# Optimization experiments

Hardware: AMD Instinct MI355X
Metric: run time of the kernel (lower is better)

The kernel has to match this reference:

```python
import jax, jax.numpy as jnp
import numpy as np
from jax.ops import segment_sum

N_NODES = 100000
N_EDGES = 1600000
IN_DIM, HID_DIM, OUT_DIM = 64, 48, 32


def setup_inputs() -> dict:
    key = jax.random.key(0)
    ks = jax.random.split(key, 4)
    x = jax.random.normal(ks[0], (N_NODES, IN_DIM), dtype=jnp.float32)
    edge_index = jax.random.randint(ks[1], (2, N_EDGES), 0, N_NODES, dtype=jnp.int64)
    W1 = jax.random.normal(ks[2], (IN_DIM, HID_DIM), dtype=jnp.float32) / np.sqrt(IN_DIM)
    b1 = jnp.zeros((HID_DIM,), dtype=jnp.float32)
    W2 = jax.random.normal(ks[3], (HID_DIM, OUT_DIM), dtype=jnp.float32) / np.sqrt(HID_DIM)
    b2 = jnp.zeros((OUT_DIM,), dtype=jnp.float32)
    return {"x": x, "edge_index": edge_index, "W1": W1, "b1": b1, "W2": W2, "b2": b2}


def _gcn_conv(x, W, b, src, dst, deg_inv_sqrt, n_nodes):
    # GCNConv: out = D^{-1/2} (A + I) D^{-1/2} (x W) + b
    h = x @ W                                   # [N, F_out]
    norm = deg_inv_sqrt[src] * deg_inv_sqrt[dst]  # [E+N]
    msg = h[src] * norm[:, None]                # gather + scale
    out = segment_sum(msg, dst, num_segments=n_nodes)  # scatter-add over dst
    return out + b


def reference(x, edge_index, W1, b1, W2, b2):
    n = x.shape[0]
    loop = jnp.arange(n, dtype=edge_index.dtype)
    src = jnp.concatenate([edge_index[0], loop])  # add self-loops (PyG default)
    dst = jnp.concatenate([edge_index[1], loop])
    deg = segment_sum(jnp.ones_like(dst, dtype=x.dtype), dst, num_segments=n)
    deg_inv_sqrt = jnp.where(deg > 0, jax.lax.rsqrt(jnp.maximum(deg, 1.0)), 0.0)
    h = _gcn_conv(x, W1, b1, src, dst, deg_inv_sqrt, n)
    h = jax.nn.relu(h)
    embeddings = _gcn_conv(h, W2, b2, src, dst, deg_inv_sqrt, n)
    return embeddings
```

## Files before the change

### kernel.cpp

```cpp
#include <hip/hip_runtime.h>
#include <hip/hip_fp16.h>


#define NN 100000
#define NE 1600000
#define NPB 128
#define NBUCK ((NN + NPB - 1) / NPB)
#define PBITS 17
#define PMASK ((1 << PBITS) - 1)
#define CHB 3
#define CHS 14
#define NKEY (NPB << CHB)
#define CAP 4096
#define UN 8
#define PART_B 512
#define EPT 8
#define PART_G ((NE + PART_B * EPT - 1) / (PART_B * EPT))
#define GROWS 256
#define GEMM_G ((NN + GROWS - 1) / GROWS)
#define GB NBUCK

struct alignas(8)  half4 { __half2 lo, hi; };
struct alignas(16) half8 { __half2 a, b, c, d; };

__global__ __launch_bounds__(512) void
k_partgemm(const int* __restrict__ src, const int* __restrict__ dst,
           int* __restrict__ cursor, int* __restrict__ packed,
           const float* __restrict__ X, const float* __restrict__ W1,
           __half* __restrict__ Hh) {
    __shared__ int h[NBUCK];
    __shared__ int base_[NBUCK];
    __shared__ float w[64 * 48];
    int tid = threadIdx.x;

    if (blockIdx.x < PART_G) {
        for (int i = tid; i < NBUCK; i += PART_B) h[i] = 0;
        __syncthreads();
        int ebase = blockIdx.x * (PART_B * EPT);
        for (int k = 0; k < EPT; ++k) {
            int e = ebase + k * PART_B + tid;
            if (e < NE) atomicAdd(&h[dst[e] >> 7], 1);
        }
        __syncthreads();
        for (int i = tid; i < NBUCK; i += PART_B) {
            int c = h[i];
            if (c) base_[i] = atomicAdd(&cursor[i], c);
            h[i] = 0;
        }
        __syncthreads();
        for (int k = 0; k < EPT; ++k) {
            int e = ebase + k * PART_B + tid;
            if (e < NE) {
                int d = dst[e];
                int b = d >> 7;
                int r = atomicAdd(&h[b], 1);
                packed[(size_t)b * CAP + base_[b] + r] = src[e] | ((d & (NPB - 1)) << PBITS);
            }
        }
        return;
    }

    constexpr int NC = 48, CPT = 12, CG = 4, KF4 = 16;
    int R0 = (blockIdx.x - PART_G) * GROWS;
    for (int i = tid; i < 64 * 48; i += 512) w[i] = W1[i];
    __syncthreads();

    int tc = tid % CG, tr = tid / CG;
    int r0 = R0 + 2 * tr, r1 = r0 + 1;
    int c0 = tc * CPT;
    bool ok0 = r0 < NN, ok1 = r1 < NN;
    const float4* X4 = (const float4*)X;
    const float4 z4 = make_float4(0.f, 0.f, 0.f, 0.f);

    float acc[2][CPT];
#pragma unroll
    for (int rr = 0; rr < 2; ++rr)
#pragma unroll
        for (int j = 0; j < CPT; ++j) acc[rr][j] = 0.f;

#pragma unroll 2
    for (int k4 = 0; k4 < KF4; ++k4) {
        float4 xa = ok0 ? X4[(size_t)r0 * KF4 + k4] : z4;
        float4 xb = ok1 ? X4[(size_t)r1 * KF4 + k4] : z4;
        float ar[4] = {xa.x, xa.y, xa.z, xa.w};
        float br[4] = {xb.x, xb.y, xb.z, xb.w};
#pragma unroll
        for (int j = 0; j < 4; ++j) {
            float va = ar[j], vb = br[j];
#pragma unroll
            for (int q = 0; q < CPT / 4; ++q) {
                float4 wv = *(const float4*)&w[(4 * k4 + j) * NC + c0 + 4 * q];
                acc[0][q*4+0] = fmaf(va, wv.x, acc[0][q*4+0]);
                acc[0][q*4+1] = fmaf(va, wv.y, acc[0][q*4+1]);
                acc[0][q*4+2] = fmaf(va, wv.z, acc[0][q*4+2]);
                acc[0][q*4+3] = fmaf(va, wv.w, acc[0][q*4+3]);
                acc[1][q*4+0] = fmaf(vb, wv.x, acc[1][q*4+0]);
                acc[1][q*4+1] = fmaf(vb, wv.y, acc[1][q*4+1]);
                acc[1][q*4+2] = fmaf(vb, wv.z, acc[1][q*4+2]);
                acc[1][q*4+3] = fmaf(vb, wv.w, acc[1][q*4+3]);
            }
        }
    }
#pragma unroll
    for (int rr = 0; rr < 2; ++rr) {
        int gr = r0 + rr;
        if (gr >= NN) continue;
#pragma unroll
        for (int q = 0; q < CPT / 4; ++q) {
            __half2 p0 = __floats2half2_rn(acc[rr][q*4+0], acc[rr][q*4+1]);
            __half2 p1 = __floats2half2_rn(acc[rr][q*4+2], acc[rr][q*4+3]);
            half4 hv; hv.lo = p0; hv.hi = p1;
            *(half4*)(Hh + (size_t)gr * NC + c0 + 4 * q) = hv;
        }
    }
}

__global__ void k_bsort(const int* __restrict__ packed, const int* __restrict__ cursor,
                        int* __restrict__ srcsort, unsigned int* __restrict__ rowinfo,
                        float* __restrict__ dinv) {
    __shared__ int stage[CAP];
    __shared__ int cnt[NKEY];
    __shared__ int tsum[256];
    int tid = threadIdx.x, b = blockIdx.x;
    int e0 = b * CAP, sz = cursor[b];
    for (int i = tid; i < NKEY; i += 256) cnt[i] = 0;
    __syncthreads();
    for (int i = tid; i < sz; i += 256) {
        int w = packed[e0 + i];
        stage[i] = w;
        int key = ((w >> PBITS) << CHB) | ((w & PMASK) >> CHS);
        atomicAdd(&cnt[key], 1);
    }
    __syncthreads();
    int k0 = tid * 4;
    int c0 = cnt[k0], c1 = cnt[k0 + 1], c2 = cnt[k0 + 2], c3 = cnt[k0 + 3];
    int loc = c0 + c1 + c2 + c3;
    tsum[tid] = loc;
    __syncthreads();
    for (int off = 1; off < 256; off <<= 1) {
        int v = (tid >= off) ? tsum[tid - off] : 0;
        __syncthreads();
        tsum[tid] += v;
        __syncthreads();
    }
    int base = tsum[tid] - loc;
    cnt[k0]     = base;
    cnt[k0 + 1] = base + c0;
    cnt[k0 + 2] = base + c0 + c1;
    cnt[k0 + 3] = base + c0 + c1 + c2;
    __syncthreads();
    if (tid < NPB) {
        int node = b * NPB + tid;
        int rs = cnt[tid << CHB];
        int re = (tid == NPB - 1) ? sz : cnt[(tid + 1) << CHB];
        if (node < NN) {
            rowinfo[node] = ((unsigned int)(e0 + rs) << 10) | (unsigned int)(re - rs);
            dinv[node] = rsqrtf((float)(re - rs + 1));
        }
    }
    __syncthreads();
    for (int i = tid; i < sz; i += 256) {
        int w = stage[i];
        int key = ((w >> PBITS) << CHB) | ((w & PMASK) >> CHS);
        int p = atomicAdd(&cnt[key], 1);
        srcsort[e0 + p] = w & PMASK;
    }
}

__global__ __launch_bounds__(256) void
k_fused48(const __half* __restrict__ Hh, const unsigned int* __restrict__ rowinfo,
          const int* __restrict__ srcsort, const float* __restrict__ dinv,
          const float* __restrict__ b1, const float* __restrict__ W2,
          __half* __restrict__ Hh2) {
    constexpr int ROWS = 128, XS = 49;
    __shared__ float Xs[ROWS * XS];
    __shared__ float w2[48 * 32];
    __shared__ float bb[48];
    int tid = threadIdx.x;
    int R0 = blockIdx.x * ROWS;
    for (int i = tid; i < 48 * 32; i += 256) w2[i] = W2[i];
    if (tid < 48) bb[tid] = b1[tid];
    __syncthreads();

    for (int t = tid; t < ROWS * 6; t += 256) {
        int lr = t / 6, q = t - lr * 6;
        int r = R0 + lr;
        if (r >= NN) continue;
        float dself = dinv[r];
        half8 sv = *(const half8*)(Hh + (size_t)r * 48 + 8 * q);
        float2 f0 = __half22float2(sv.a), f1 = __half22float2(sv.b);
        float2 f2 = __half22float2(sv.c), f3 = __half22float2(sv.d);
        float a0 = f0.x * dself, a1 = f0.y * dself;
        float a2 = f1.x * dself, a3 = f1.y * dself;
        float a4 = f2.x * dself, a5 = f2.y * dself;
        float a6 = f3.x * dself, a7 = f3.y * dself;
        unsigned int rp = rowinfo[r];
        int e0 = rp >> 10, e1 = e0 + (int)(rp & 1023);
        for (int e = e0; e < e1; e += UN) {
            int ss[UN]; float ms[UN];
#pragma unroll
            for (int u = 0; u < UN; ++u) {
                int ee = e + u;
                bool ok = ee < e1;
                ss[u] = srcsort[ok ? ee : e0];
                ms[u] = ok ? 1.f : 0.f;
            }
            half8 vv[UN]; float dv[UN];
#pragma unroll
            for (int u = 0; u < UN; ++u) {
                vv[u] = *(const half8*)(Hh + (size_t)ss[u] * 48 + 8 * q);
                dv[u] = dinv[ss[u]];
            }
#pragma unroll
            for (int u = 0; u < UN; ++u) {
                float2 g0 = __half22float2(vv[u].a), g1 = __half22float2(vv[u].b);
                float2 g2 = __half22float2(vv[u].c), g3 = __half22float2(vv[u].d);
                float m = ms[u] * dv[u];
                a0 = fmaf(g0.x, m, a0); a1 = fmaf(g0.y, m, a1);
                a2 = fmaf(g1.x, m, a2); a3 = fmaf(g1.y, m, a3);
                a4 = fmaf(g2.x, m, a4); a5 = fmaf(g2.y, m, a5);
                a6 = fmaf(g3.x, m, a6); a7 = fmaf(g3.y, m, a7);
            }
        }
        float d = dself;
        float* xr = &Xs[lr * XS + 8 * q];
        const float* bf = &bb[8 * q];
        xr[0] = fmaxf(fmaf(a0, d, bf[0]), 0.f);
        xr[1] = fmaxf(fmaf(a1, d, bf[1]), 0.f);
        xr[2] = fmaxf(fmaf(a2, d, bf[2]), 0.f);
        xr[3] = fmaxf(fmaf(a3, d, bf[3]), 0.f);
        xr[4] = fmaxf(fmaf(a4, d, bf[4]), 0.f);
        xr[5] = fmaxf(fmaf(a5, d, bf[5]), 0.f);
        xr[6] = fmaxf(fmaf(a6, d, bf[6]), 0.f);
        xr[7] = fmaxf(fmaf(a7, d, bf[7]), 0.f);
    }
    __syncthreads();

    int tc = tid & 3, tr = tid >> 2;
    int r0l = 2 * tr, c0 = tc * 8;
    float acc[2][8];
#pragma unroll
    for (int rr = 0; rr < 2; ++rr)
#pragma unroll
        for (int j = 0; j < 8; ++j) acc[rr][j] = 0.f;
#pragma unroll 4
    for (int k = 0; k < 48; ++k) {
        float x0 = Xs[r0l * XS + k];
        float x1 = Xs[(r0l + 1) * XS + k];
        float4 wv0 = *(const float4*)&w2[k * 32 + c0];
        float4 wv1 = *(const float4*)&w2[k * 32 + c0 + 4];
        acc[0][0] = fmaf(x0, wv0.x, acc[0][0]); acc[0][1] = fmaf(x0, wv0.y, acc[0][1]);
        acc[0][2] = fmaf(x0, wv0.z, acc[0][2]); acc[0][3] = fmaf(x0, wv0.w, acc[0][3]);
        acc[0][4] = fmaf(x0, wv1.x, acc[0][4]); acc[0][5] = fmaf(x0, wv1.y, acc[0][5]);
        acc[0][6] = fmaf(x0, wv1.z, acc[0][6]); acc[0][7] = fmaf(x0, wv1.w, acc[0][7]);
        acc[1][0] = fmaf(x1, wv0.x, acc[1][0]); acc[1][1] = fmaf(x1, wv0.y, acc[1][1]);
        acc[1][2] = fmaf(x1, wv0.z, acc[1][2]); acc[1][3] = fmaf(x1, wv0.w, acc[1][3]);
        acc[1][4] = fmaf(x1, wv1.x, acc[1][4]); acc[1][5] = fmaf(x1, wv1.y, acc[1][5]);
        acc[1][6] = fmaf(x1, wv1.z, acc[1][6]); acc[1][7] = fmaf(x1, wv1.w, acc[1][7]);
    }
#pragma unroll
    for (int rr = 0; rr < 2; ++rr) {
        int gr = R0 + r0l + rr;
        if (gr >= NN) continue;
        float d = dinv[gr];
        __half2 p0 = __floats2half2_rn(acc[rr][0] * d, acc[rr][1] * d);
        __half2 p1 = __floats2half2_rn(acc[rr][2] * d, acc[rr][3] * d);
        __half2 p2 = __floats2half2_rn(acc[rr][4] * d, acc[rr][5] * d);
        __half2 p3 = __floats2half2_rn(acc[rr][6] * d, acc[rr][7] * d);
        half8 hv; hv.a = p0; hv.b = p1; hv.c = p2; hv.d = p3;
        *(half8*)(Hh2 + (size_t)gr * 32 + c0) = hv;
    }
}

template <int NC>
__global__ void k_agg(const __half* __restrict__ Hh, const unsigned int* __restrict__ rowinfo,
                      const int* __restrict__ srcsort, const float* __restrict__ dinv,
                      const float* __restrict__ bias, float* __restrict__ out) {
    constexpr int Q = NC / 8;
    int idx = blockIdx.x * blockDim.x + threadIdx.x;
    if (idx >= NN * Q) return;
    int r = idx / Q, q = idx - r * Q;
    half8 sv = *(const half8*)(Hh + (size_t)r * NC + 8 * q);
    float2 f0 = __half22float2(sv.a), f1 = __half22float2(sv.b);
    float2 f2 = __half22float2(sv.c), f3 = __half22float2(sv.d);
    float a0 = f0.x, a1 = f0.y, a2 = f1.x, a3 = f1.y;
    float a4 = f2.x, a5 = f2.y, a6 = f3.x, a7 = f3.y;
    unsigned int rp = rowinfo[r];
    int e0 = rp >> 10, e1 = e0 + (int)(rp & 1023);
    for (int e = e0; e < e1; e += UN) {
        int ss[UN]; float ms[UN];
#pragma unroll
        for (int u = 0; u < UN; ++u) {
            int ee = e + u;
            bool ok = ee < e1;
            ss[u] = srcsort[ok ? ee : e0];
            ms[u] = ok ? 1.f : 0.f;
        }
        half8 vv[UN];
#pragma unroll
        for (int u = 0; u < UN; ++u)
            vv[u] = *(const half8*)(Hh + (size_t)ss[u] * NC + 8 * q);
#pragma unroll
        for (int u = 0; u < UN; ++u) {
            float2 g0 = __half22float2(vv[u].a), g1 = __half22float2(vv[u].b);
            float2 g2 = __half22float2(vv[u].c), g3 = __half22float2(vv[u].d);
            float m = ms[u];
            a0 = fmaf(g0.x, m, a0); a1 = fmaf(g0.y, m, a1);
            a2 = fmaf(g1.x, m, a2); a3 = fmaf(g1.y, m, a3);
            a4 = fmaf(g2.x, m, a4); a5 = fmaf(g2.y, m, a5);
            a6 = fmaf(g3.x, m, a6); a7 = fmaf(g3.y, m, a7);
        }
    }
    float d = dinv[r];
    const float4* b4 = (const float4*)bias;
    float4 bv0 = b4[2 * q], bv1 = b4[2 * q + 1];
    a0 = fmaf(a0, d, bv0.x); a1 = fmaf(a1, d, bv0.y);
    a2 = fmaf(a2, d, bv0.z); a3 = fmaf(a3, d, bv0.w);
    a4 = fmaf(a4, d, bv1.x); a5 = fmaf(a5, d, bv1.y);
    a6 = fmaf(a6, d, bv1.z); a7 = fmaf(a7, d, bv1.w);
    float4* o4 = (float4*)(out + (size_t)r * NC + 8 * q);
    o4[0] = make_float4(a0, a1, a2, a3);
    o4[1] = make_float4(a4, a5, a6, a7);
}

extern "C" void kernel_launch(void* const* d_in, const int* in_sizes, int n_in,
                              void* d_out, int out_size, void* d_ws, size_t ws_size,
                              hipStream_t stream) {
    const float* x  = (const float*)d_in[0];
    const int*   ei = (const int*)d_in[1];
    const float* W1 = (const float*)d_in[2];
    const float* b1 = (const float*)d_in[3];
    const float* W2 = (const float*)d_in[4];
    const float* b2 = (const float*)d_in[5];
    float* out = (float*)d_out;

    const int* src = ei;
    const int* dst = ei + NE;

    char* p = (char*)d_ws;
    auto take = [&](size_t elems) { void* q = p; p += ((elems * 4 + 255) & ~255ull); return q; };
    int*          cursor  = (int*)take(NBUCK);
    unsigned int* rowinfo = (unsigned int*)take(NN);
    float*        dinv    = (float*)take(NN);
    int*          srcsort = (int*)take((size_t)NBUCK * CAP);
    __half*       Hh      = (__half*)take((size_t)NN * 24);
    int*          packed  = (int*)take((size_t)NBUCK * CAP);
    __half*       Hh2     = (__half*)packed;

    const int B = 256;
    hipMemsetAsync(cursor, 0, NBUCK * sizeof(int), stream);
    k_partgemm<<<PART_G + GEMM_G, 512, 0, stream>>>(src, dst, cursor, packed, x, W1, Hh);
    k_bsort<<<NBUCK, 256, 0, stream>>>(packed, cursor, srcsort, rowinfo, dinv);
    k_fused48<<<GB, 256, 0, stream>>>(Hh, rowinfo, srcsort, dinv, b1, W2, Hh2);
    k_agg<32><<<(NN * 4 + B - 1) / B, B, 0, stream>>>(Hh2, rowinfo, srcsort, dinv, b2, out);
}
```

Baseline: 205.9 us.

## Replace atomic bucket scatter with per-block local sort runs and segment merge

The partition kernel no longer reserves space with global atomics on a bucket cursor and scatters each edge to a random global slot. Each block now sorts its edges by bucket locally in shared memory, writes them out as one contiguous run, and records a per-bucket offset and length table. The bucket-sort kernel then gathers its bucket's segments from all runs into shared memory before the counting sort. This removes the global atomics, the memset and the scattered writes, but each bucket block now makes many short serial per-thread segment reads, and the new seg table adds extra memory traffic.

```diff
diff --git a/kernel.cpp b/kernel.cpp
--- a/kernel.cpp
+++ b/kernel.cpp
@@ -15,7 +15,8 @@
 #define UN 8
 #define PART_B 512
 #define EPT 8
-#define PART_G ((NE + PART_B * EPT - 1) / (PART_B * EPT))
+#define RUNW (PART_B * EPT)
+#define PART_G ((NE + RUNW - 1) / RUNW)
 #define GROWS 256
 #define GEMM_G ((NN + GROWS - 1) / GROWS)
 #define GB NBUCK
@@ -24,39 +25,62 @@
 struct alignas(16) half8 { __half2 a, b, c, d; };
 
 __global__ __launch_bounds__(512) void
-k_partgemm(const int* __restrict__ src, const int* __restrict__ dst,
-           int* __restrict__ cursor, int* __restrict__ packed,
-           const float* __restrict__ X, const float* __restrict__ W1,
-           __half* __restrict__ Hh) {
+k_lsortgemm(const int* __restrict__ src, const int* __restrict__ dst,
+            int* __restrict__ runs, unsigned int* __restrict__ seg,
+            const float* __restrict__ X, const float* __restrict__ W1,
+            __half* __restrict__ Hh) {
     __shared__ int h[NBUCK];
-    __shared__ int base_[NBUCK];
+    __shared__ int tsum[512];
+    __shared__ int stage[RUNW];
     __shared__ float w[64 * 48];
     int tid = threadIdx.x;
 
     if (blockIdx.x < PART_G) {
         for (int i = tid; i < NBUCK; i += PART_B) h[i] = 0;
         __syncthreads();
-        int ebase = blockIdx.x * (PART_B * EPT);
-        for (int k = 0; k < EPT; ++k) {
-            int e = ebase + k * PART_B + tid;
-            if (e < NE) atomicAdd(&h[dst[e] >> 7], 1);
-        }
-        __syncthreads();
-        for (int i = tid; i < NBUCK; i += PART_B) {
-            int c = h[i];
-            if (c) base_[i] = atomicAdd(&cursor[i], c);
-            h[i] = 0;
-        }
-        __syncthreads();
+        int ebase = blockIdx.x * RUNW;
+        int pw[EPT], pb[EPT];
+#pragma unroll
         for (int k = 0; k < EPT; ++k) {
             int e = ebase + k * PART_B + tid;
             if (e < NE) {
                 int d = dst[e];
-                int b = d >> 7;
-                int r = atomicAdd(&h[b], 1);
-                packed[(size_t)b * CAP + base_[b] + r] = src[e] | ((d & (NPB - 1)) << PBITS);
+                pb[k] = d >> 7;
+                pw[k] = src[e] | ((d & (NPB - 1)) << PBITS);
+                atomicAdd(&h[pb[k]], 1);
+            } else pb[k] = -1;
+        }
+        __syncthreads();
+        int c0 = 0, c1 = 0;
+        if (tid < NBUCK / 2) { c0 = h[2 * tid]; c1 = h[2 * tid + 1]; }
+        int loc = c0 + c1;
+        tsum[tid] = (tid < NBUCK / 2) ? loc : 0;
+        __syncthreads();
+        for (int off = 1; off < 512; off <<= 1) {
+            int v = (tid >= off) ? tsum[tid - off] : 0;
+            __syncthreads();
+            tsum[tid] += v;
+            __syncthreads();
+        }
+        if (tid < NBUCK / 2) {
+            int base = tsum[tid] - loc;
+            seg[(size_t)blockIdx.x * NBUCK + 2 * tid]     = ((unsigned)base << 9) | (unsigned)c0;
+            seg[(size_t)blockIdx.x * NBUCK + 2 * tid + 1] = ((unsigned)(base + c0) << 9) | (unsigned)c1;
+            h[2 * tid]     = base;
+            h[2 * tid + 1] = base + c0;
+        }
+        __syncthreads();
+#pragma unroll
+        for (int k = 0; k < EPT; ++k) {
+            if (pb[k] >= 0) {
+                int r = atomicAdd(&h[pb[k]], 1);
+                stage[r] = pw[k];
             }
         }
+        __syncthreads();
+#pragma unroll
+        for (int k = 0; k < EPT; ++k)
+            runs[(size_t)blockIdx.x * RUNW + k * PART_B + tid] = stage[k * PART_B + tid];
         return;
     }
 
@@ -115,19 +139,40 @@
     }
 }
 
-__global__ void k_bsort(const int* __restrict__ packed, const int* __restrict__ cursor,
-                        int* __restrict__ srcsort, unsigned int* __restrict__ rowinfo,
-                        float* __restrict__ dinv) {
+__global__ __launch_bounds__(256) void
+k_bsort2(const int* __restrict__ runs, const unsigned int* __restrict__ seg,
+         int* __restrict__ srcsort, unsigned int* __restrict__ rowinfo,
+         float* __restrict__ dinv) {
     __shared__ int stage[CAP];
     __shared__ int cnt[NKEY];
     __shared__ int tsum[256];
     int tid = threadIdx.x, b = blockIdx.x;
-    int e0 = b * CAP, sz = cursor[b];
+
+    unsigned int s0 = (tid < PART_G) ? seg[(size_t)tid * NBUCK + b] : 0u;
+    unsigned int s1 = (tid + 256 < PART_G) ? seg[(size_t)(tid + 256) * NBUCK + b] : 0u;
+    int l0 = (int)(s0 & 511u), l1 = (int)(s1 & 511u);
+    int mylen = l0 + l1;
+    tsum[tid] = mylen;
+    __syncthreads();
+    for (int off = 1; off < 256; off <<= 1) {
+        int v = (tid >= off) ? tsum[tid - off] : 0;
+        __syncthreads();
+        tsum[tid] += v;
+        __syncthreads();
+    }
+    int wbase = tsum[tid] - mylen;
+    int sz = tsum[255];
+    {
+        const int* p = runs + (size_t)tid * RUNW + (s0 >> 9);
+        for (int i = 0; i < l0; ++i) stage[wbase + i] = p[i];
+        p = runs + (size_t)(tid + 256) * RUNW + (s1 >> 9);
+        for (int i = 0; i < l1; ++i) stage[wbase + l0 + i] = p[i];
+    }
     for (int i = tid; i < NKEY; i += 256) cnt[i] = 0;
     __syncthreads();
+
     for (int i = tid; i < sz; i += 256) {
-        int w = packed[e0 + i];
-        stage[i] = w;
+        int w = stage[i];
         int key = ((w >> PBITS) << CHB) | ((w & PMASK) >> CHS);
         atomicAdd(&cnt[key], 1);
     }
@@ -149,6 +194,7 @@
     cnt[k0 + 2] = base + c0 + c1;
     cnt[k0 + 3] = base + c0 + c1 + c2;
     __syncthreads();
+    int e0 = b * CAP;
     if (tid < NPB) {
         int node = b * NPB + tid;
         int rs = cnt[tid << CHB];
@@ -339,18 +385,17 @@
 
     char* p = (char*)d_ws;
     auto take = [&](size_t elems) { void* q = p; p += ((elems * 4 + 255) & ~255ull); return q; };
-    int*          cursor  = (int*)take(NBUCK);
     unsigned int* rowinfo = (unsigned int*)take(NN);
     float*        dinv    = (float*)take(NN);
     int*          srcsort = (int*)take((size_t)NBUCK * CAP);
     __half*       Hh      = (__half*)take((size_t)NN * 24);
-    int*          packed  = (int*)take((size_t)NBUCK * CAP);
-    __half*       Hh2     = (__half*)packed;
+    unsigned int* seg     = (unsigned int*)take((size_t)PART_G * NBUCK);
+    int*          runs    = (int*)take((size_t)PART_G * RUNW);
+    __half*       Hh2     = (__half*)runs;
 
     const int B = 256;
-    hipMemsetAsync(cursor, 0, NBUCK * sizeof(int), stream);
-    k_partgemm<<<PART_G + GEMM_G, 512, 0, stream>>>(src, dst, cursor, packed, x, W1, Hh);
-    k_bsort<<<NBUCK, 256, 0, stream>>>(packed, cursor, srcsort, rowinfo, dinv);
+    k_lsortgemm<<<PART_G + GEMM_G, PART_B, 0, stream>>>(src, dst, runs, seg, x, W1, Hh);
+    k_bsort2<<<NBUCK, 256, 0, stream>>>(runs, seg, srcsort, rowinfo, dinv);
     k_fused48<<<GB, 256, 0, stream>>>(Hh, rowinfo, srcsort, dinv, b1, W2, Hh2);
     k_agg<32><<<(NN * 4 + B - 1) / B, B, 0, stream>>>(Hh2, rowinfo, srcsort, dinv, b2, out);
 }
```

Measured after the change: 200.5 us. 1.03x faster.
